# Kernel tuning notes

Measured on AMD Instinct MI355X. Metric: run time of the kernel, lower is better.

## Reference

```python
import jax, jax.numpy as jnp
import numpy as np

B, N, C, H = 4, 2048, 2048, 16
DH = C // H  # 128


def setup_inputs() -> dict:
    key = jax.random.key(0)
    ks = jax.random.split(key, 5)
    s = 0.02
    return {
        "x": jax.random.normal(ks[0], (B, N, C), dtype=jnp.float32),
        "w_qkv": jax.random.normal(ks[1], (3 * C, C), dtype=jnp.float32) * s,
        "b_qkv": jax.random.normal(ks[2], (3 * C,), dtype=jnp.float32) * s,
        "w_out": jax.random.normal(ks[3], (C, C), dtype=jnp.float32) * s,
        "b_out": jax.random.normal(ks[4], (C,), dtype=jnp.float32) * s,
    }


def reference(x, w_qkv, b_qkv, w_out, b_out):
    b, n, c = x.shape
    # fused QKV projection (torch Linear: x @ W.T + b)
    qkv = x @ w_qkv.T + b_qkv                      # (B, N, 3C)
    qkv = qkv.reshape(b, n, 3, H, c // H)          # (B, N, 3, H, Dh)
    q, k, v = qkv[:, :, 0], qkv[:, :, 1], qkv[:, :, 2]  # each (B, N, H, Dh)
    # NOTE: faithful to source — no transpose(1,2), so attention mixes HEADS
    # per token: attn has shape (B, N, H, H), scale is 1/sqrt(C).
    attn = jnp.einsum("bnhd,bngd->bnhg", q, k) / jnp.sqrt(jnp.float32(c))
    attn = jax.nn.softmax(attn, axis=-1)
    out = jnp.einsum("bnhg,bngd->bnhd", attn, v)   # (B, N, H, Dh)
    # faithful to source: transpose(1,2) then reshape (interleaves h and n)
    out = out.transpose(0, 2, 1, 3).reshape(b, n, c)
    return out @ w_out.T + b_out
```

## Files before the change

kernel.cpp:

```cpp
#include <hip/hip_runtime.h>

typedef unsigned short u16;
typedef unsigned int u32;
typedef __bf16 bf16x8 __attribute__((ext_vector_type(8)));
typedef float f32x4 __attribute__((ext_vector_type(4)));
typedef float f32x16 __attribute__((ext_vector_type(16)));


__device__ __forceinline__ u16 f2bf(float f) {
    u32 u = __builtin_bit_cast(u32, f);
    u += 0x7FFFu + ((u >> 16) & 1u);
    return (u16)(u >> 16);
}
__device__ __forceinline__ float bf2f(u16 h) {
    return __builtin_bit_cast(float, ((u32)h) << 16);
}

__global__ __launch_bounds__(256) void cvt_bf16(const float* __restrict__ in,
                                                u16* __restrict__ out, int n4) {
    int i = blockIdx.x * 256 + threadIdx.x;
    if (i >= n4) return;
    const float4 f = reinterpret_cast<const float4*>(in)[i];
    ushort4 o;
    o.x = f2bf(f.x); o.y = f2bf(f.y); o.z = f2bf(f.z); o.w = f2bf(f.w);
    reinterpret_cast<ushort4*>(out)[i] = o;
}

typedef const __attribute__((address_space(1))) void* gas1_t;
typedef __attribute__((address_space(3))) void* las3_t;
__device__ __forceinline__ void cp16(const void* g, void* l) {
    __builtin_amdgcn_global_load_lds((gas1_t)g, (las3_t)l, 16, 0, 0);
}

template <int OUT_BF16>
__global__ __launch_bounds__(256) void gemm_nt(const u16* __restrict__ A,
                                               const u16* __restrict__ Bm,
                                               const float* __restrict__ bias,
                                               void* __restrict__ Cout,
                                               int M, int N, int K) {
    __shared__ __align__(16) u16 lA[2][128 * 32];
    __shared__ __align__(16) u16 lB[2][128 * 32];

    const int tid  = threadIdx.x;
    const int lane = tid & 63;
    const int wave = tid >> 6;
    const int wm   = (wave >> 1) * 64;
    const int wn   = (wave & 1) * 64;
    const int r32  = lane & 31;
    const int half = lane >> 5;

    const long bm = (long)blockIdx.y * 128;
    const long bn = (long)blockIdx.x * 128;

    f32x16 acc[2][2];
#pragma unroll
    for (int i = 0; i < 2; ++i)
#pragma unroll
        for (int j = 0; j < 2; ++j)
#pragma unroll
            for (int r = 0; r < 16; ++r) acc[i][j][r] = 0.f;

    const int srow = tid >> 2;
    const int sq   = (tid & 3) ^ ((srow >> 1) & 3);
    const u16* ga = A  + (bm + srow) * (long)K + sq * 8;
    const u16* gb = Bm + (bn + srow) * (long)K + sq * 8;
    u16* la0 = &lA[0][tid * 8];
    u16* lb0 = &lB[0][tid * 8];
    u16* la1 = &lA[1][tid * 8];
    u16* lb1 = &lB[1][tid * 8];
    const long hK = 64 * (long)K;

    const int xr = (r32 >> 1) & 3;
    const int q0 = (0 + half) ^ xr;
    const int q1 = (2 + half) ^ xr;

    cp16(ga, la0);
    cp16(ga + hK, la0 + 64 * 32);
    cp16(gb, lb0);
    cp16(gb + hK, lb0 + 64 * 32);
    __syncthreads();

    int cur = 0;
    for (int k0 = 32; k0 < K; k0 += 32) {
        u16* la = cur ? la0 : la1;
        u16* lb = cur ? lb0 : lb1;
        cp16(ga + k0, la);
        cp16(ga + k0 + hK, la + 64 * 32);
        cp16(gb + k0, lb);
        cp16(gb + k0 + hK, lb + 64 * 32);

        const u16* cA = lA[cur];
        const u16* cB = lB[cur];
        bf16x8 af[2][2], bf[2][2];
#pragma unroll
        for (int t = 0; t < 2; ++t) {
            const int rowA = (wm + t * 32 + r32) * 32;
            const int rowB = (wn + t * 32 + r32) * 32;
            af[t][0] = *reinterpret_cast<const bf16x8*>(&cA[rowA + q0 * 8]);
            af[t][1] = *reinterpret_cast<const bf16x8*>(&cA[rowA + q1 * 8]);
            bf[t][0] = *reinterpret_cast<const bf16x8*>(&cB[rowB + q0 * 8]);
            bf[t][1] = *reinterpret_cast<const bf16x8*>(&cB[rowB + q1 * 8]);
        }

#pragma unroll
        for (int ks = 0; ks < 2; ++ks)
#pragma unroll
            for (int i = 0; i < 2; ++i)
#pragma unroll
                for (int j = 0; j < 2; ++j)
                    acc[i][j] = __builtin_amdgcn_mfma_f32_32x32x16_bf16(af[i][ks], bf[j][ks], acc[i][j], 0, 0, 0);

        __syncthreads();
        cur ^= 1;
    }

    {
        const u16* cA = lA[cur];
        const u16* cB = lB[cur];
        bf16x8 af[2][2], bf[2][2];
#pragma unroll
        for (int t = 0; t < 2; ++t) {
            const int rowA = (wm + t * 32 + r32) * 32;
            const int rowB = (wn + t * 32 + r32) * 32;
            af[t][0] = *reinterpret_cast<const bf16x8*>(&cA[rowA + q0 * 8]);
            af[t][1] = *reinterpret_cast<const bf16x8*>(&cA[rowA + q1 * 8]);
            bf[t][0] = *reinterpret_cast<const bf16x8*>(&cB[rowB + q0 * 8]);
            bf[t][1] = *reinterpret_cast<const bf16x8*>(&cB[rowB + q1 * 8]);
        }
#pragma unroll
        for (int ks = 0; ks < 2; ++ks)
#pragma unroll
            for (int i = 0; i < 2; ++i)
#pragma unroll
                for (int j = 0; j < 2; ++j)
                    acc[i][j] = __builtin_amdgcn_mfma_f32_32x32x16_bf16(af[i][ks], bf[j][ks], acc[i][j], 0, 0, 0);
    }

#pragma unroll
    for (int j = 0; j < 2; ++j) {
        const long col = bn + wn + j * 32 + r32;
        const float bc = bias[col];
#pragma unroll
        for (int i = 0; i < 2; ++i) {
#pragma unroll
            for (int reg = 0; reg < 16; ++reg) {
                const long row = bm + wm + i * 32 + (reg & 3) + 8 * (reg >> 2) + 4 * half;
                float v = acc[i][j][reg] + bc;
                if (OUT_BF16)
                    ((u16*)Cout)[row * (long)N + col] = f2bf(v);
                else
                    ((float*)Cout)[row * (long)N + col] = v;
            }
        }
    }
}

__global__ __launch_bounds__(256) void attn(const u16* __restrict__ qkv,
                                            u16* __restrict__ outb) {
    __shared__ float sQ[16 * 132];
    __shared__ float sK[16 * 132];
    __shared__ float sV[16 * 132];
    __shared__ float sP[16 * 17];

    const int tid = threadIdx.x;
    const int token = blockIdx.x;
    const int b = token >> 11;
    const int n = token & 2047;
    const u16* row = qkv + (long)token * 6144;

    {
        const int r  = tid >> 4;
        const int c8 = (tid & 15) * 8;
#pragma unroll
        for (int m = 0; m < 3; ++m) {
            const uint4 u = *reinterpret_cast<const uint4*>(row + m * 2048 + tid * 8);
            float* dst = (m == 0 ? sQ : (m == 1 ? sK : sV)) + r * 132 + c8;
            float4 lo, hi;
            lo.x = bf2f((u16)u.x); lo.y = bf2f((u16)(u.x >> 16));
            lo.z = bf2f((u16)u.y); lo.w = bf2f((u16)(u.y >> 16));
            hi.x = bf2f((u16)u.z); hi.y = bf2f((u16)(u.z >> 16));
            hi.z = bf2f((u16)u.w); hi.w = bf2f((u16)(u.w >> 16));
            *reinterpret_cast<float4*>(dst)     = lo;
            *reinterpret_cast<float4*>(dst + 4) = hi;
        }
    }
    __syncthreads();

    {
        const int h = tid >> 4, g = tid & 15;
        const float4* qr = reinterpret_cast<const float4*>(&sQ[h * 132]);
        const float4* kr = reinterpret_cast<const float4*>(&sK[g * 132]);
        float s = 0.f;
#pragma unroll
        for (int d = 0; d < 32; ++d) {
            const float4 a = qr[d], k4 = kr[d];
            s += a.x * k4.x + a.y * k4.y + a.z * k4.z + a.w * k4.w;
        }
        s *= 0.022097086912079608f;
        float mx = s;
#pragma unroll
        for (int o = 8; o >= 1; o >>= 1) mx = fmaxf(mx, __shfl_xor(mx, o, 16));
        const float e = __expf(s - mx);
        float sum = e;
#pragma unroll
        for (int o = 8; o >= 1; o >>= 1) sum += __shfl_xor(sum, o, 16);
        sP[h * 17 + g] = e / sum;
    }
    __syncthreads();

    {
        const int h = tid >> 4, dblk = tid & 15;
        float p[16];
#pragma unroll
        for (int g = 0; g < 16; ++g) p[g] = sP[h * 17 + g];
        float4 o0 = {0.f, 0.f, 0.f, 0.f}, o1 = {0.f, 0.f, 0.f, 0.f};
#pragma unroll
        for (int g = 0; g < 16; ++g) {
            const float* vr = &sV[g * 132 + dblk * 8];
            const float4 v0 = *reinterpret_cast<const float4*>(vr);
            const float4 v1 = *reinterpret_cast<const float4*>(vr + 4);
            o0.x += p[g] * v0.x; o0.y += p[g] * v0.y; o0.z += p[g] * v0.z; o0.w += p[g] * v0.w;
            o1.x += p[g] * v1.x; o1.y += p[g] * v1.y; o1.z += p[g] * v1.z; o1.w += p[g] * v1.w;
        }
        const long rr = (long)h * 128 + (n >> 4);
        const long cc = (long)(n & 15) * 128 + dblk * 8;
        u16* dst = outb + ((long)b * 2048 + rr) * 2048 + cc;
        uint4 pk;
        pk.x = (u32)f2bf(o0.x) | ((u32)f2bf(o0.y) << 16);
        pk.y = (u32)f2bf(o0.z) | ((u32)f2bf(o0.w) << 16);
        pk.z = (u32)f2bf(o1.x) | ((u32)f2bf(o1.y) << 16);
        pk.w = (u32)f2bf(o1.z) | ((u32)f2bf(o1.w) << 16);
        *reinterpret_cast<uint4*>(dst) = pk;
    }
}

extern "C" void kernel_launch(void* const* d_in, const int* in_sizes, int n_in,
                              void* d_out, int out_size, void* d_ws, size_t ws_size,
                              hipStream_t stream) {
    const float* x     = (const float*)d_in[0];
    const float* w_qkv = (const float*)d_in[1];
    const float* b_qkv = (const float*)d_in[2];
    const float* w_out = (const float*)d_in[3];
    const float* b_out = (const float*)d_in[4];
    float* out = (float*)d_out;

    char* ws = (char*)d_ws;
    u16* xb    = (u16*)(ws);
    u16* wqkvb = (u16*)(ws + 33554432);
    u16* woutb = (u16*)(ws + 58720256);
    u16* qkvb  = (u16*)(ws + 67108864);
    u16* attnb = xb;

    cvt_bf16<<<16384, 256, 0, stream>>>(x,     xb,    16777216 / 4);
    cvt_bf16<<<12288, 256, 0, stream>>>(w_qkv, wqkvb, 12582912 / 4);
    cvt_bf16<<<4096,  256, 0, stream>>>(w_out, woutb, 4194304 / 4);

    dim3 g1(48, 64);
    gemm_nt<1><<<g1, 256, 0, stream>>>(xb, wqkvb, b_qkv, qkvb, 8192, 6144, 2048);

    attn<<<8192, 256, 0, stream>>>(qkvb, attnb);

    dim3 g2(16, 64);
    gemm_nt<0><<<g2, 256, 0, stream>>>(attnb, woutb, b_out, out, 8192, 2048, 2048);
}
```

Before: 541.9 us.

## Rewrite GEMM as 256x256 tile, 8-wave kernel with interleaved LDS prefetch

Replaces the 128x128, 4-wave, double-buffered GEMM with a 256x256 tile and 512 threads. It uses 16x16x32 MFMAs, 64-deep K tiles and a hand-scheduled interleave of global-to-LDS copies with MFMA quadrants, controlled by explicit vmcnt/lgkmcnt waits and s_setprio. The aim is more data reuse per LDS byte and better overlap of memory with matrix math in both projection GEMMs. The cost is 128KB of LDS, heavy register pressure, and fewer blocks per CU (256 blocks for the output GEMM), which may hurt occupancy and wave balance.

```diff
diff --git a/kernel.cpp b/kernel.cpp
--- a/kernel.cpp
+++ b/kernel.cpp
@@ -4,7 +4,6 @@
 typedef unsigned int u32;
 typedef __bf16 bf16x8 __attribute__((ext_vector_type(8)));
 typedef float f32x4 __attribute__((ext_vector_type(4)));
-typedef float f32x16 __attribute__((ext_vector_type(16)));
 
 
 __device__ __forceinline__ u16 f2bf(float f) {
@@ -32,120 +31,153 @@
     __builtin_amdgcn_global_load_lds((gas1_t)g, (las3_t)l, 16, 0, 0);
 }
 
+#define BAR()        __builtin_amdgcn_s_barrier()
+#define WAIT_LGKM0() asm volatile("s_waitcnt lgkmcnt(0)" ::: "memory")
+#define WAIT_VM6()   asm volatile("s_waitcnt vmcnt(6)" ::: "memory")
+#define WAIT_VM0()   asm volatile("s_waitcnt vmcnt(0)" ::: "memory")
+
+
+__device__ __forceinline__ void ld_a4(bf16x8 (&a)[4][2], const char* rdA, int off, int mt0) {
+#pragma unroll
+    for (int i = 0; i < 4; ++i) {
+        a[i][0] = *(const bf16x8*)(rdA + off +        (mt0 + i) * 256);
+        a[i][1] = *(const bf16x8*)(rdA + off + 8192 + (mt0 + i) * 256);
+    }
+}
+__device__ __forceinline__ void ld_b2(bf16x8 (&b)[4][2], const char* rdB, int off, int nt0) {
+#pragma unroll
+    for (int j = 0; j < 2; ++j) {
+        b[nt0 + j][0] = *(const bf16x8*)(rdB + off +        (nt0 + j) * 256);
+        b[nt0 + j][1] = *(const bf16x8*)(rdB + off + 8192 + (nt0 + j) * 256);
+    }
+}
+
+template <int MH, int NH>
+__device__ __forceinline__ void mfma_quad(f32x4 (&acc)[8][4], bf16x8 (&a)[4][2], bf16x8 (&b)[4][2]) {
+    __builtin_amdgcn_s_setprio(1);
+#pragma unroll
+    for (int ks = 0; ks < 2; ++ks)
+#pragma unroll
+        for (int i = 0; i < 4; ++i)
+#pragma unroll
+            for (int j = 0; j < 2; ++j)
+                acc[MH * 4 + i][NH * 2 + j] = __builtin_amdgcn_mfma_f32_16x16x32_bf16(
+                    a[i][ks], b[NH * 2 + j][ks], acc[MH * 4 + i][NH * 2 + j], 0, 0, 0);
+    __builtin_amdgcn_s_setprio(0);
+}
+
 template <int OUT_BF16>
-__global__ __launch_bounds__(256) void gemm_nt(const u16* __restrict__ A,
-                                               const u16* __restrict__ Bm,
-                                               const float* __restrict__ bias,
-                                               void* __restrict__ Cout,
-                                               int M, int N, int K) {
-    __shared__ __align__(16) u16 lA[2][128 * 32];
-    __shared__ __align__(16) u16 lB[2][128 * 32];
+__global__ __launch_bounds__(512, 2) void gemm_nt(const u16* __restrict__ A,
+                                                  const u16* __restrict__ Bm,
+                                                  const float* __restrict__ bias,
+                                                  void* __restrict__ Cout,
+                                                  int M, int N, int K) {
+    __shared__ __align__(16) char lds[131072];
 
     const int tid  = threadIdx.x;
     const int lane = tid & 63;
     const int wave = tid >> 6;
-    const int wm   = (wave >> 1) * 64;
-    const int wn   = (wave & 1) * 64;
-    const int r32  = lane & 31;
-    const int half = lane >> 5;
-
-    const long bm = (long)blockIdx.y * 128;
-    const long bn = (long)blockIdx.x * 128;
-
-    f32x16 acc[2][2];
-#pragma unroll
-    for (int i = 0; i < 2; ++i)
-#pragma unroll
-        for (int j = 0; j < 2; ++j)
-#pragma unroll
-            for (int r = 0; r < 16; ++r) acc[i][j][r] = 0.f;
-
-    const int srow = tid >> 2;
-    const int sq   = (tid & 3) ^ ((srow >> 1) & 3);
-    const u16* ga = A  + (bm + srow) * (long)K + sq * 8;
-    const u16* gb = Bm + (bn + srow) * (long)K + sq * 8;
-    u16* la0 = &lA[0][tid * 8];
-    u16* lb0 = &lB[0][tid * 8];
-    u16* la1 = &lA[1][tid * 8];
-    u16* lb1 = &lB[1][tid * 8];
-    const long hK = 64 * (long)K;
-
-    const int xr = (r32 >> 1) & 3;
-    const int q0 = (0 + half) ^ xr;
-    const int q1 = (2 + half) ^ xr;
-
-    cp16(ga, la0);
-    cp16(ga + hK, la0 + 64 * 32);
-    cp16(gb, lb0);
-    cp16(gb + hK, lb0 + 64 * 32);
-    __syncthreads();
-
-    int cur = 0;
-    for (int k0 = 32; k0 < K; k0 += 32) {
-        u16* la = cur ? la0 : la1;
-        u16* lb = cur ? lb0 : lb1;
-        cp16(ga + k0, la);
-        cp16(ga + k0 + hK, la + 64 * 32);
-        cp16(gb + k0, lb);
-        cp16(gb + k0 + hK, lb + 64 * 32);
-
-        const u16* cA = lA[cur];
-        const u16* cB = lB[cur];
-        bf16x8 af[2][2], bf[2][2];
-#pragma unroll
-        for (int t = 0; t < 2; ++t) {
-            const int rowA = (wm + t * 32 + r32) * 32;
-            const int rowB = (wn + t * 32 + r32) * 32;
-            af[t][0] = *reinterpret_cast<const bf16x8*>(&cA[rowA + q0 * 8]);
-            af[t][1] = *reinterpret_cast<const bf16x8*>(&cA[rowA + q1 * 8]);
-            bf[t][0] = *reinterpret_cast<const bf16x8*>(&cB[rowB + q0 * 8]);
-            bf[t][1] = *reinterpret_cast<const bf16x8*>(&cB[rowB + q1 * 8]);
-        }
-
-#pragma unroll
-        for (int ks = 0; ks < 2; ++ks)
-#pragma unroll
-            for (int i = 0; i < 2; ++i)
-#pragma unroll
-                for (int j = 0; j < 2; ++j)
-                    acc[i][j] = __builtin_amdgcn_mfma_f32_32x32x16_bf16(af[i][ks], bf[j][ks], acc[i][j], 0, 0, 0);
-
-        __syncthreads();
-        cur ^= 1;
-    }
-
-    {
-        const u16* cA = lA[cur];
-        const u16* cB = lB[cur];
-        bf16x8 af[2][2], bf[2][2];
-#pragma unroll
-        for (int t = 0; t < 2; ++t) {
-            const int rowA = (wm + t * 32 + r32) * 32;
-            const int rowB = (wn + t * 32 + r32) * 32;
-            af[t][0] = *reinterpret_cast<const bf16x8*>(&cA[rowA + q0 * 8]);
-            af[t][1] = *reinterpret_cast<const bf16x8*>(&cA[rowA + q1 * 8]);
-            bf[t][0] = *reinterpret_cast<const bf16x8*>(&cB[rowB + q0 * 8]);
-            bf[t][1] = *reinterpret_cast<const bf16x8*>(&cB[rowB + q1 * 8]);
-        }
-#pragma unroll
-        for (int ks = 0; ks < 2; ++ks)
-#pragma unroll
-            for (int i = 0; i < 2; ++i)
-#pragma unroll
-                for (int j = 0; j < 2; ++j)
-                    acc[i][j] = __builtin_amdgcn_mfma_f32_32x32x16_bf16(af[i][ks], bf[j][ks], acc[i][j], 0, 0, 0);
-    }
-
-#pragma unroll
-    for (int j = 0; j < 2; ++j) {
-        const long col = bn + wn + j * 32 + r32;
+    const int wm   = wave >> 2;
+    const int wn   = wave & 3;
+    const int l16  = lane & 15;
+    const int kg   = lane >> 4;
+
+    const long bm = (long)blockIdx.y * 256;
+    const long bn = (long)blockIdx.x * 256;
+
+    const int srow = tid & 127;
+    const int skc  = tid >> 7;
+    const u16* gA0 = A  + (bm + srow) * (long)K + skc * 8;
+    const u16* gA1 = gA0 + 128 * (long)K;
+    const u16* gB0 = Bm + (bn + srow) * (long)K + skc * 8;
+    const u16* gB1 = gB0 + 128 * (long)K;
+    char* ldst = lds + tid * 16;
+
+#define STAGE_A(HALF, BUF, KT)                                    \
+    { const u16* g = ((HALF) ? gA1 : gA0) + (KT) * 64;            \
+      char* d = ldst + (BUF) * 32768 + (HALF) * 16384;            \
+      cp16(g, d); cp16(g + 32, d + 8192); }
+#define STAGE_B(HALF, BUF, KT)                                    \
+    { const u16* g = ((HALF) ? gB1 : gB0) + (KT) * 64;            \
+      char* d = ldst + 65536 + (BUF) * 32768 + (HALF) * 16384;    \
+      cp16(g, d); cp16(g + 32, d + 8192); }
+
+    const char* rdA = lds + wm * 16384 + kg * 2048 + l16 * 16;
+    const char* rdB = lds + 65536 + (wn >> 1) * 16384 + kg * 2048
+                      + ((wn & 1) * 64 + l16) * 16;
+
+    f32x4 acc[8][4];
+#pragma unroll
+    for (int i = 0; i < 8; ++i)
+#pragma unroll
+        for (int j = 0; j < 4; ++j)
+#pragma unroll
+            for (int r = 0; r < 4; ++r) acc[i][j][r] = 0.f;
+
+    const int NT = K >> 6;
+
+    STAGE_B(0, 0, 0); STAGE_B(1, 0, 0); STAGE_A(0, 0, 0); STAGE_A(1, 0, 0);
+    STAGE_B(0, 1, 1); STAGE_B(1, 1, 1); STAGE_A(0, 1, 1);
+    WAIT_VM6();
+    BAR();
+
+    bf16x8 a[4][2], b[4][2];
+
+#define KTILE(RBUF, A1B, A1K, BB, BKT, A0B, A0K)                  \
+    {                                                             \
+        const int ro = (RBUF) * 32768;                            \
+                                     \
+        ld_a4(a, rdA, ro, 0);                                     \
+        ld_b2(b, rdB, ro, 0);                                     \
+        STAGE_A(1, A1B, A1K);                                     \
+        BAR(); WAIT_LGKM0();                                      \
+        mfma_quad<0, 0>(acc, a, b);                               \
+        BAR();                                                    \
+                                     \
+        ld_b2(b, rdB, ro, 2);                                     \
+        BAR(); WAIT_LGKM0();                                      \
+        mfma_quad<0, 1>(acc, a, b);                               \
+        BAR();                                                    \
+                                     \
+        ld_a4(a, rdA, ro, 4);                                     \
+        STAGE_B(0, BB, BKT); STAGE_B(1, BB, BKT);                 \
+        BAR(); WAIT_LGKM0();                                      \
+        mfma_quad<1, 0>(acc, a, b);                               \
+        BAR();                                                    \
+                                     \
+        STAGE_A(0, A0B, A0K);                                     \
+        BAR(); WAIT_LGKM0();                                      \
+        mfma_quad<1, 1>(acc, a, b);                               \
+        WAIT_VM6();                                               \
+        BAR();                                                    \
+    }
+
+    const int NIT = NT >> 1;
+    for (int it = 0; it < NIT; ++it) {
+        const int T = 2 * it;
+        int t2 = T + 2; if (t2 >= NT) t2 -= NT;
+        int t3 = T + 3; if (t3 >= NT) t3 -= NT;
+        KTILE(0, 1, T + 1, 0, t2, 0, t2);
+        KTILE(1, 0, t2,    1, t3, 1, t3);
+    }
+#undef KTILE
+#undef STAGE_A
+#undef STAGE_B
+
+    WAIT_VM0();
+
+    const long crow0 = bm + wm * 128;
+    const long ccol0 = bn + wn * 64 + l16;
+#pragma unroll
+    for (int nt = 0; nt < 4; ++nt) {
+        const long col = ccol0 + nt * 16;
         const float bc = bias[col];
 #pragma unroll
-        for (int i = 0; i < 2; ++i) {
-#pragma unroll
-            for (int reg = 0; reg < 16; ++reg) {
-                const long row = bm + wm + i * 32 + (reg & 3) + 8 * (reg >> 2) + 4 * half;
-                float v = acc[i][j][reg] + bc;
+        for (int mt = 0; mt < 8; ++mt) {
+#pragma unroll
+            for (int r = 0; r < 4; ++r) {
+                const long row = crow0 + mt * 16 + kg * 4 + r;
+                float v = acc[mt][nt][r] + bc;
                 if (OUT_BF16)
                     ((u16*)Cout)[row * (long)N + col] = f2bf(v);
                 else
@@ -255,11 +287,11 @@
     cvt_bf16<<<12288, 256, 0, stream>>>(w_qkv, wqkvb, 12582912 / 4);
     cvt_bf16<<<4096,  256, 0, stream>>>(w_out, woutb, 4194304 / 4);
 
-    dim3 g1(48, 64);
-    gemm_nt<1><<<g1, 256, 0, stream>>>(xb, wqkvb, b_qkv, qkvb, 8192, 6144, 2048);
+    dim3 g1(24, 32);
+    gemm_nt<1><<<g1, 512, 0, stream>>>(xb, wqkvb, b_qkv, qkvb, 8192, 6144, 2048);
 
     attn<<<8192, 256, 0, stream>>>(qkvb, attnb);
 
-    dim3 g2(16, 64);
-    gemm_nt<0><<<g2, 256, 0, stream>>>(attnb, woutb, b_out, out, 8192, 2048, 2048);
-}
+    dim3 g2(8, 32);
+    gemm_nt<0><<<g2, 512, 0, stream>>>(attnb, woutb, b_out, out, 8192, 2048, 2048);
+}
```

Result: no change. 540.1 us (-0.3%).

## Deepen GEMM pipeline to four LDS stages with manual waitcnt and tile swizzle

Applied to the files above, without the earlier changes.

Replaces the double-buffered GEMM main loop with a four-stage LDS ring. Three tiles are prefetched ahead, and a raw s_waitcnt vmcnt plus a bare barrier replace __syncthreads. The LDS layout changes to a k-chunk-major arrangement without the XOR swizzle. Blocks are remapped across the grid for L2 locality, and MFMA priority is raised with s_setprio. The goal is to hide global-load latency and cut barrier cost, at the price of 64KB of LDS per block and possible LDS bank conflicts. The loop also issues wrapped, redundant loads for the last tiles.

```diff
diff --git a/kernel.cpp b/kernel.cpp
--- a/kernel.cpp
+++ b/kernel.cpp
@@ -3,7 +3,6 @@
 typedef unsigned short u16;
 typedef unsigned int u32;
 typedef __bf16 bf16x8 __attribute__((ext_vector_type(8)));
-typedef float f32x4 __attribute__((ext_vector_type(4)));
 typedef float f32x16 __attribute__((ext_vector_type(16)));
 
 
@@ -32,14 +31,18 @@
     __builtin_amdgcn_global_load_lds((gas1_t)g, (las3_t)l, 16, 0, 0);
 }
 
+#define BAR()        __builtin_amdgcn_s_barrier()
+#define SBAR0()      __builtin_amdgcn_sched_barrier(0)
+#define WAIT_VM(n)   asm volatile("s_waitcnt vmcnt(" #n ")" ::: "memory")
+
+
 template <int OUT_BF16>
-__global__ __launch_bounds__(256) void gemm_nt(const u16* __restrict__ A,
-                                               const u16* __restrict__ Bm,
-                                               const float* __restrict__ bias,
-                                               void* __restrict__ Cout,
-                                               int M, int N, int K) {
-    __shared__ __align__(16) u16 lA[2][128 * 32];
-    __shared__ __align__(16) u16 lB[2][128 * 32];
+__global__ __launch_bounds__(256, 2) void gemm_nt(const u16* __restrict__ A,
+                                                  const u16* __restrict__ Bm,
+                                                  const float* __restrict__ bias,
+                                                  void* __restrict__ Cout,
+                                                  int M, int N, int K) {
+    __shared__ __align__(16) char lds[4 * 16384];
 
     const int tid  = threadIdx.x;
     const int lane = tid & 63;
@@ -49,8 +52,27 @@
     const int r32  = lane & 31;
     const int half = lane >> 5;
 
-    const long bm = (long)blockIdx.y * 128;
-    const long bn = (long)blockIdx.x * 128;
+    const int gx   = gridDim.x;
+    const int flat = blockIdx.y * gx + blockIdx.x;
+    const int q8   = (gx * gridDim.y) >> 3;
+    const int swz  = (flat & 7) * q8 + (flat >> 3);
+    const long bm  = (long)(swz / gx) * 128;
+    const long bn  = (long)(swz % gx) * 128;
+
+    const int sr  = tid & 127;
+    const int skc = tid >> 7;
+    const u16* gA = A  + (bm + sr) * (long)K + skc * 8;
+    const u16* gB = Bm + (bn + sr) * (long)K + skc * 8;
+    char* ld0 = lds + tid * 16;
+
+#define STAGE(BUF, KT)                                              \
+    { const long ko = (long)(KT) * 32;                              \
+      char* d = ld0 + (BUF) * 16384;                                \
+      cp16(gA + ko, d);      cp16(gA + ko + 16, d + 4096);          \
+      cp16(gB + ko, d + 8192); cp16(gB + ko + 16, d + 12288); }
+
+    const char* pA = lds + half * 2048 + (wm + r32) * 16;
+    const char* pB = lds + 8192 + half * 2048 + (wn + r32) * 16;
 
     f32x16 acc[2][2];
 #pragma unroll
@@ -60,81 +82,44 @@
 #pragma unroll
             for (int r = 0; r < 16; ++r) acc[i][j][r] = 0.f;
 
-    const int srow = tid >> 2;
-    const int sq   = (tid & 3) ^ ((srow >> 1) & 3);
-    const u16* ga = A  + (bm + srow) * (long)K + sq * 8;
-    const u16* gb = Bm + (bn + srow) * (long)K + sq * 8;
-    u16* la0 = &lA[0][tid * 8];
-    u16* lb0 = &lB[0][tid * 8];
-    u16* la1 = &lA[1][tid * 8];
-    u16* lb1 = &lB[1][tid * 8];
-    const long hK = 64 * (long)K;
-
-    const int xr = (r32 >> 1) & 3;
-    const int q0 = (0 + half) ^ xr;
-    const int q1 = (2 + half) ^ xr;
-
-    cp16(ga, la0);
-    cp16(ga + hK, la0 + 64 * 32);
-    cp16(gb, lb0);
-    cp16(gb + hK, lb0 + 64 * 32);
-    __syncthreads();
-
-    int cur = 0;
-    for (int k0 = 32; k0 < K; k0 += 32) {
-        u16* la = cur ? la0 : la1;
-        u16* lb = cur ? lb0 : lb1;
-        cp16(ga + k0, la);
-        cp16(ga + k0 + hK, la + 64 * 32);
-        cp16(gb + k0, lb);
-        cp16(gb + k0 + hK, lb + 64 * 32);
-
-        const u16* cA = lA[cur];
-        const u16* cB = lB[cur];
-        bf16x8 af[2][2], bf[2][2];
-#pragma unroll
-        for (int t = 0; t < 2; ++t) {
-            const int rowA = (wm + t * 32 + r32) * 32;
-            const int rowB = (wn + t * 32 + r32) * 32;
-            af[t][0] = *reinterpret_cast<const bf16x8*>(&cA[rowA + q0 * 8]);
-            af[t][1] = *reinterpret_cast<const bf16x8*>(&cA[rowA + q1 * 8]);
-            bf[t][0] = *reinterpret_cast<const bf16x8*>(&cB[rowB + q0 * 8]);
-            bf[t][1] = *reinterpret_cast<const bf16x8*>(&cB[rowB + q1 * 8]);
-        }
-
+    const int NT = K >> 5;
+
+    STAGE(0, 0); STAGE(1, 1); STAGE(2, 2);
+    WAIT_VM(8);
+    BAR(); SBAR0();
+
+#pragma unroll 4
+    for (int t = 0; t < NT; ++t) {
+        int kt = t + 3; if (kt >= NT) kt -= NT;
+        STAGE((t + 3) & 3, kt);
+
+        const int bo = (t & 3) * 16384;
+        bf16x8 a[2][2], b[2][2];
 #pragma unroll
         for (int ks = 0; ks < 2; ++ks)
 #pragma unroll
+            for (int u = 0; u < 2; ++u) {
+                a[u][ks] = *(const bf16x8*)(pA + bo + ks * 4096 + u * 512);
+                b[u][ks] = *(const bf16x8*)(pB + bo + ks * 4096 + u * 512);
+            }
+
+        __builtin_amdgcn_s_setprio(1);
+#pragma unroll
+        for (int ks = 0; ks < 2; ++ks)
+#pragma unroll
             for (int i = 0; i < 2; ++i)
 #pragma unroll
                 for (int j = 0; j < 2; ++j)
-                    acc[i][j] = __builtin_amdgcn_mfma_f32_32x32x16_bf16(af[i][ks], bf[j][ks], acc[i][j], 0, 0, 0);
-
-        __syncthreads();
-        cur ^= 1;
-    }
-
-    {
-        const u16* cA = lA[cur];
-        const u16* cB = lB[cur];
-        bf16x8 af[2][2], bf[2][2];
-#pragma unroll
-        for (int t = 0; t < 2; ++t) {
-            const int rowA = (wm + t * 32 + r32) * 32;
-            const int rowB = (wn + t * 32 + r32) * 32;
-            af[t][0] = *reinterpret_cast<const bf16x8*>(&cA[rowA + q0 * 8]);
-            af[t][1] = *reinterpret_cast<const bf16x8*>(&cA[rowA + q1 * 8]);
-            bf[t][0] = *reinterpret_cast<const bf16x8*>(&cB[rowB + q0 * 8]);
-            bf[t][1] = *reinterpret_cast<const bf16x8*>(&cB[rowB + q1 * 8]);
-        }
-#pragma unroll
-        for (int ks = 0; ks < 2; ++ks)
-#pragma unroll
-            for (int i = 0; i < 2; ++i)
-#pragma unroll
-                for (int j = 0; j < 2; ++j)
-                    acc[i][j] = __builtin_amdgcn_mfma_f32_32x32x16_bf16(af[i][ks], bf[j][ks], acc[i][j], 0, 0, 0);
-    }
+                    acc[i][j] = __builtin_amdgcn_mfma_f32_32x32x16_bf16(
+                        a[i][ks], b[j][ks], acc[i][j], 0, 0, 0);
+        __builtin_amdgcn_s_setprio(0);
+
+        WAIT_VM(8);
+        BAR(); SBAR0();
+    }
+#undef STAGE
+
+    WAIT_VM(0);
 
 #pragma unroll
     for (int j = 0; j < 2; ++j) {
```

After: 788.8 us. 1.46x slower.
